# Performance work log

Hardware: AMD Instinct MI355X
Metric: run time of the kernel (lower is better)

## Reference

```python
import jax, jax.numpy as jnp
import numpy as np


def setup_inputs() -> dict:
    key = jax.random.key(0)
    ks = jax.random.split(key, 6)
    B, Din, Dout, K, L = 4096, 4096, 4096, 256, 4
    # scale params like kaiming-ish init to keep activations O(1)
    hin = jax.random.normal(ks[0], (B, Din), dtype=jnp.float32)
    S1s = jax.random.normal(ks[1], (L, Din, K), dtype=jnp.float32) / np.sqrt(Din)
    S2s = jax.random.normal(ks[2], (L, K, Dout), dtype=jnp.float32) / np.sqrt(K)
    U1s = jax.random.normal(ks[3], (L, K, Dout), dtype=jnp.float32) / np.sqrt(K)
    U2s = jax.random.normal(ks[4], (L, Din, K), dtype=jnp.float32) / np.sqrt(Din)
    bias = jax.random.normal(ks[5], (Dout,), dtype=jnp.float32)
    return {"hin": hin, "S1s": S1s, "S2s": S2s, "U1s": U1s, "U2s": U2s, "bias": bias}


def reference(hin, S1s, S2s, U1s, U2s, bias):
    # out = (sum_l (hin @ S1s_l @ U1s_l + hin @ U2s_l @ S2s_l) + bias) / (2 L)
    L = S1s.shape[0]
    a = jnp.einsum('bd,ldk->lbk', hin, S1s)      # [L, B, K]
    t1 = jnp.einsum('lbk,lko->bo', a, U1s)       # [B, Dout]
    b = jnp.einsum('bd,ldk->lbk', hin, U2s)      # [L, B, K]
    t2 = jnp.einsum('lbk,lko->bo', b, S2s)       # [B, Dout]
    return (t1 + t2 + bias) / (2.0 * L)
```

## Files before the change

### kernel.cpp

```cpp
#include <hip/hip_runtime.h>
#include <stdint.h>

typedef unsigned short u16;
typedef __bf16 bf16x8 __attribute__((ext_vector_type(8)));
typedef float f32x4 __attribute__((ext_vector_type(4)));

#define DIN 4096
#define DOUT 4096
#define BB 4096
#define KR 256
#define RK 2048

__device__ __forceinline__ u16 f2bf(float f) {
    union { float f; unsigned u; } v; v.f = f;
    unsigned r = v.u + 0x7FFFu + ((v.u >> 16) & 1u);
    return (u16)(r >> 16);
}

__device__ __forceinline__ void gl_lds16(const void* g, void* l) {
    __builtin_amdgcn_global_load_lds((const __attribute__((address_space(1))) void*)g,
                                     (__attribute__((address_space(3))) void*)l,
                                     16, 0, 0);
}

__global__ __launch_bounds__(256) void cvt_f32_bf16(const float* __restrict__ src,
                                                    u16* __restrict__ dst, int n8) {
    int i = blockIdx.x * blockDim.x + threadIdx.x;
    if (i >= n8) return;
    const float4* s = reinterpret_cast<const float4*>(src) + (size_t)i * 2;
    float4 a = s[0], b = s[1];
    uint4 o;
    o.x = f2bf(a.x) | ((unsigned)f2bf(a.y) << 16);
    o.y = f2bf(a.z) | ((unsigned)f2bf(a.w) << 16);
    o.z = f2bf(b.x) | ((unsigned)f2bf(b.y) << 16);
    o.w = f2bf(b.z) | ((unsigned)f2bf(b.w) << 16);
    reinterpret_cast<uint4*>(dst)[i] = o;
}

__global__ __launch_bounds__(256) void pack_w1t(const float* __restrict__ S1s,
                                                const float* __restrict__ U2s,
                                                u16* __restrict__ W1T) {
    __shared__ u16 lds[64][68];
    int b  = blockIdx.x;
    int bd = b & 63;
    int bk = (b >> 6) & 3;
    int lb = b >> 8;
    int l = lb >> 1, br = lb & 1;
    const float* src = (br ? U2s : S1s) + (size_t)l * DIN * KR;
    int t = threadIdx.x;
    int d0 = bd * 64, k0 = bk * 64;
    int r0 = l * 512 + br * 256 + k0;
    #pragma unroll
    for (int p = 0; p < 4; ++p) {
        int dl = p * 16 + (t >> 4);
        int kc = (t & 15) * 4;
        float4 v = *reinterpret_cast<const float4*>(src + (size_t)(d0 + dl) * KR + k0 + kc);
        ushort4 pk;
        pk.x = f2bf(v.x); pk.y = f2bf(v.y); pk.z = f2bf(v.z); pk.w = f2bf(v.w);
        *reinterpret_cast<ushort4*>(&lds[dl][kc]) = pk;
    }
    __syncthreads();
    #pragma unroll
    for (int p = 0; p < 2; ++p) {
        int kl = p * 32 + (t >> 3);
        int d8 = t & 7;
        u16 tmp[8];
        #pragma unroll
        for (int j = 0; j < 8; ++j) tmp[j] = lds[d8 * 8 + j][kl];
        uint4 o;
        o.x = tmp[0] | ((unsigned)tmp[1] << 16);
        o.y = tmp[2] | ((unsigned)tmp[3] << 16);
        o.z = tmp[4] | ((unsigned)tmp[5] << 16);
        o.w = tmp[6] | ((unsigned)tmp[7] << 16);
        *reinterpret_cast<uint4*>(W1T + (size_t)(r0 + kl) * DIN + d0 + d8 * 8) = o;
    }
}

__global__ __launch_bounds__(256) void pack_w2t(const float* __restrict__ U1s,
                                                const float* __restrict__ S2s,
                                                u16* __restrict__ W2T) {
    __shared__ u16 lds[64][68];
    int b  = blockIdx.x;
    int bo = b & 63;
    int bk = (b >> 6) & 3;
    int lb = b >> 8;
    int l = lb >> 1, br = lb & 1;
    const float* src = (br ? S2s : U1s) + (size_t)l * KR * DOUT;
    int t = threadIdx.x;
    int o0 = bo * 64, k0 = bk * 64;
    #pragma unroll
    for (int p = 0; p < 4; ++p) {
        int kl = p * 16 + (t >> 4);
        int ol = (t & 15) * 4;
        float4 v = *reinterpret_cast<const float4*>(src + (size_t)(k0 + kl) * DOUT + o0 + ol);
        ushort4 pk;
        pk.x = f2bf(v.x); pk.y = f2bf(v.y); pk.z = f2bf(v.z); pk.w = f2bf(v.w);
        *reinterpret_cast<ushort4*>(&lds[kl][ol]) = pk;
    }
    __syncthreads();
    #pragma unroll
    for (int p = 0; p < 2; ++p) {
        int ol = p * 32 + (t >> 3);
        int k8 = t & 7;
        u16 tmp[8];
        #pragma unroll
        for (int j = 0; j < 8; ++j) tmp[j] = lds[k8 * 8 + j][ol];
        uint4 o;
        o.x = tmp[0] | ((unsigned)tmp[1] << 16);
        o.y = tmp[2] | ((unsigned)tmp[3] << 16);
        o.z = tmp[4] | ((unsigned)tmp[5] << 16);
        o.w = tmp[6] | ((unsigned)tmp[7] << 16);
        *reinterpret_cast<uint4*>(W2T + (size_t)(o0 + ol) * RK + l * 512 + br * 256 + k0 + k8 * 8) = o;
    }
}

template <int BN, int EPI>
__global__ __launch_bounds__(512) void gemm8(const u16* __restrict__ A,
                                             const u16* __restrict__ Bt,
                                             void* __restrict__ Cv,
                                             const float* __restrict__ bias,
                                             int N, int Kd) {
    extern __shared__ char smem[];
    constexpr int BHB = (BN == 256) ? 16384 : 8192;
    constexpr int BROWS = BN / 2;
    constexpr int NF = BN / 128;
    char* ldsA = smem;
    char* ldsB = smem + 65536;

    const int tid = threadIdx.x;
    const int l = tid & 63;
    const int wv = tid >> 6;
    const int wr = wv >> 2;
    const int wc = wv & 3;

    int bid = blockIdx.x;
    bid = (bid & 7) * 32 + (bid >> 3);
    const int mt = bid >> 4, nt = bid & 15;
    const int m0 = mt * 256, n0 = nt * BN;

    const int NITER = Kd >> 7;

    size_t aoff[2], boff[2];
    {
        #pragma unroll
        for (int r = 0; r < 2; ++r) {
            int lin = (r * 512 + tid) * 16;
            int s = lin ^ (((lin >> 7) & 7) << 4);
            int e = s >> 1;
            size_t o = (size_t)(e >> 6) * Kd + (e & 63);
            aoff[r] = (size_t)m0 * Kd + o;
            boff[r] = (size_t)n0 * Kd + o;
        }
    }

    auto issueA = [&](int h, int b, size_t kb) {
        char* d = ldsA + (((b << 1) | h) * 16384) + tid * 16;
        gl_lds16(A + aoff[0] + (size_t)h * 128 * Kd + kb, d);
        gl_lds16(A + aoff[1] + (size_t)h * 128 * Kd + kb, d + 8192);
    };
    auto issueB = [&](int h, int b, size_t kb) {
        char* d = ldsB + (((b << 1) | h) * BHB) + tid * 16;
        gl_lds16(Bt + boff[0] + (size_t)h * BROWS * Kd + kb, d);
        if constexpr (BN == 256)
            gl_lds16(Bt + boff[1] + (size_t)h * BROWS * Kd + kb, d + 8192);
    };

    int rowAb[4];
    #pragma unroll
    for (int m = 0; m < 4; ++m) rowAb[m] = (wr * 64 + m * 16 + (l & 15)) * 128;
    int rowBb[NF];
    #pragma unroll
    for (int n = 0; n < NF; ++n)
        rowBb[n] = ((BN == 256 ? wc * 32 : wc * 16) + n * 16 + (l & 15)) * 128;
    const int cc0 = ((l >> 4) ^ (l & 7)) << 4;

    f32x4 acc[2][2][4][NF] = {};

#define PHASE(BUF, MH, NH, ISSUE_STMT, VM) do {                                   \
    bf16x8 af_[4][2]; bf16x8 bq_[NF][2];                                          \
    const char* Ah_ = ldsA + (((BUF) << 1) | (MH)) * 16384;                       \
    const char* Bh_ = ldsB + (((BUF) << 1) | (NH)) * BHB;                         \
    _Pragma("unroll") for (int m_ = 0; m_ < 4; ++m_) {                            \
        af_[m_][0] = *(const bf16x8*)(Ah_ + (rowAb[m_] | cc0));                   \
        af_[m_][1] = *(const bf16x8*)(Ah_ + ((rowAb[m_] | cc0) ^ 64)); }          \
    _Pragma("unroll") for (int n_ = 0; n_ < NF; ++n_) {                           \
        bq_[n_][0] = *(const bf16x8*)(Bh_ + (rowBb[n_] | cc0));                   \
        bq_[n_][1] = *(const bf16x8*)(Bh_ + ((rowBb[n_] | cc0) ^ 64)); }          \
    ISSUE_STMT;                                                                   \
    __builtin_amdgcn_s_barrier();                                                 \
    asm volatile("s_waitcnt lgkmcnt(0)" ::: "memory");                            \
    __builtin_amdgcn_s_setprio(1);                                                \
    _Pragma("unroll") for (int m_ = 0; m_ < 4; ++m_)                              \
        _Pragma("unroll") for (int n_ = 0; n_ < NF; ++n_) {                       \
            acc[MH][NH][m_][n_] = __builtin_amdgcn_mfma_f32_16x16x32_bf16(        \
                af_[m_][0], bq_[n_][0], acc[MH][NH][m_][n_], 0, 0, 0);            \
            acc[MH][NH][m_][n_] = __builtin_amdgcn_mfma_f32_16x16x32_bf16(        \
                af_[m_][1], bq_[n_][1], acc[MH][NH][m_][n_], 0, 0, 0); }          \
    __builtin_amdgcn_s_setprio(0);                                                \
    if (VM) { if (BN == 256) asm volatile("s_waitcnt vmcnt(4)" ::: "memory");     \
              else           asm volatile("s_waitcnt vmcnt(3)" ::: "memory"); }   \
    __builtin_amdgcn_s_barrier();                                                 \
} while (0)

    issueA(0, 0, 0);  issueB(0, 0, 0);
    issueA(1, 0, 0);  issueB(1, 0, 0);
    issueA(0, 1, 64); issueB(0, 1, 64);
    if (BN == 256) asm volatile("s_waitcnt vmcnt(4)" ::: "memory");
    else           asm volatile("s_waitcnt vmcnt(3)" ::: "memory");
    __builtin_amdgcn_s_barrier();

    for (int J = 0; J < NITER; ++J) {
        const size_t kc = (size_t)J << 7;
        PHASE(0, 0, 0, issueA(1, 1, kc + 64),  0);
        PHASE(0, 0, 1, issueB(1, 1, kc + 64),  0);
        PHASE(0, 1, 0, issueA(0, 0, kc + 128), 0);
        PHASE(0, 1, 1, issueB(0, 0, kc + 128), 1);
        PHASE(1, 0, 0, issueA(1, 0, kc + 128), 0);
        PHASE(1, 0, 1, issueB(1, 0, kc + 128), 0);
        PHASE(1, 1, 0, issueA(0, 1, kc + 192), 0);
        PHASE(1, 1, 1, issueB(0, 1, kc + 192), 1);
    }
#undef PHASE

    const int colc = l & 15, rb = (l >> 4) * 4;
    #pragma unroll
    for (int mh = 0; mh < 2; ++mh)
    #pragma unroll
    for (int nh = 0; nh < 2; ++nh)
    #pragma unroll
    for (int m = 0; m < 4; ++m)
    #pragma unroll
    for (int n = 0; n < NF; ++n) {
        int c = n0 + nh * (BN / 2) + wc * (BN / 8) + n * 16 + colc;
        int r0r = m0 + mh * 128 + wr * 64 + m * 16 + rb;
        if (EPI == 0) {
            u16* Cb = (u16*)Cv;
            #pragma unroll
            for (int j = 0; j < 4; ++j)
                Cb[(size_t)(r0r + j) * N + c] = f2bf(acc[mh][nh][m][n][j]);
        } else {
            float* Cf = (float*)Cv;
            float bv = bias[c];
            #pragma unroll
            for (int j = 0; j < 4; ++j)
                Cf[(size_t)(r0r + j) * N + c] = (acc[mh][nh][m][n][j] + bv) * 0.125f;
        }
    }
}

extern "C" void kernel_launch(void* const* d_in, const int* in_sizes, int n_in,
                              void* d_out, int out_size, void* d_ws, size_t ws_size,
                              hipStream_t stream) {
    const float* hin  = (const float*)d_in[0];
    const float* S1s  = (const float*)d_in[1];
    const float* S2s  = (const float*)d_in[2];
    const float* U1s  = (const float*)d_in[3];
    const float* U2s  = (const float*)d_in[4];
    const float* bias = (const float*)d_in[5];
    float* out = (float*)d_out;

    const size_t SZ_HIN = (size_t)BB * DIN * 2 + 512;
    const size_t SZ_W   = (size_t)RK * DIN * 2 + 512;
    const size_t SZ_A   = (size_t)BB * RK * 2 + 512;
    if (ws_size < SZ_HIN + SZ_W + SZ_A) return;
    u16* hinbf = (u16*)d_ws;
    u16* Wx    = (u16*)((char*)d_ws + SZ_HIN);
    u16* abf   = (u16*)((char*)d_ws + SZ_HIN + SZ_W);

    (void)hipFuncSetAttribute(reinterpret_cast<const void*>(&gemm8<128, 0>),
                              hipFuncAttributeMaxDynamicSharedMemorySize, 98304);
    (void)hipFuncSetAttribute(reinterpret_cast<const void*>(&gemm8<256, 1>),
                              hipFuncAttributeMaxDynamicSharedMemorySize, 131072);

    pack_w1t<<<64 * 4 * 8, 256, 0, stream>>>(S1s, U2s, Wx);
    cvt_f32_bf16<<<(BB * DIN / 8) / 256, 256, 0, stream>>>(hin, hinbf, BB * DIN / 8);
    gemm8<128, 0><<<256, 512, 98304, stream>>>(hinbf, Wx, abf, nullptr, RK, DIN);
    pack_w2t<<<64 * 4 * 8, 256, 0, stream>>>(U1s, S2s, Wx);
    gemm8<256, 1><<<256, 512, 131072, stream>>>(abf, Wx, out, bias, DOUT, RK);
}
```

Measured before the change: 189.0 us.

## Reshape wave tiling and reuse A/B LDS fragments across consecutive phases

Makes the per-wave layout configurable (MW waves along M) so each wave computes a tile 2 fragments wide in N. Fragment registers are hoisted out of the phase so A fragments are reused across the two N-halves and B fragments across the M-halves. The phase order is changed to 00,01,11,10 so consecutive phases share one operand. This cuts LDS read traffic per MFMA but raises register pressure, since B fragments for both N-halves stay live.

```diff
diff --git a/kernel.cpp b/kernel.cpp
--- a/kernel.cpp
+++ b/kernel.cpp
@@ -114,7 +114,7 @@
     }
 }
 
-template <int BN, int EPI>
+template <int BN, int MW, int EPI>
 __global__ __launch_bounds__(512) void gemm8(const u16* __restrict__ A,
                                              const u16* __restrict__ Bt,
                                              void* __restrict__ Cv,
@@ -123,15 +123,17 @@
     extern __shared__ char smem[];
     constexpr int BHB = (BN == 256) ? 16384 : 8192;
     constexpr int BROWS = BN / 2;
-    constexpr int NF = BN / 128;
+    constexpr int NW = 8 / MW;
+    constexpr int MF = 128 / (16 * MW);
+    constexpr int MROW = 128 / MW;
     char* ldsA = smem;
     char* ldsB = smem + 65536;
 
     const int tid = threadIdx.x;
     const int l = tid & 63;
     const int wv = tid >> 6;
-    const int wr = wv >> 2;
-    const int wc = wv & 3;
+    const int wr = wv / NW;
+    const int wc = wv % NW;
 
     int bid = blockIdx.x;
     bid = (bid & 7) * 32 + (bid >> 3);
@@ -165,37 +167,37 @@
             gl_lds16(Bt + boff[1] + (size_t)h * BROWS * Kd + kb, d + 8192);
     };
 
-    int rowAb[4];
-    #pragma unroll
-    for (int m = 0; m < 4; ++m) rowAb[m] = (wr * 64 + m * 16 + (l & 15)) * 128;
-    int rowBb[NF];
-    #pragma unroll
-    for (int n = 0; n < NF; ++n)
-        rowBb[n] = ((BN == 256 ? wc * 32 : wc * 16) + n * 16 + (l & 15)) * 128;
+    int rowAb[MF];
+    #pragma unroll
+    for (int m = 0; m < MF; ++m) rowAb[m] = (wr * MROW + m * 16 + (l & 15)) * 128;
+    int rowBb[2];
+    #pragma unroll
+    for (int n = 0; n < 2; ++n) rowBb[n] = (wc * 32 + n * 16 + (l & 15)) * 128;
     const int cc0 = ((l >> 4) ^ (l & 7)) << 4;
 
-    f32x4 acc[2][2][4][NF] = {};
-
-#define PHASE(BUF, MH, NH, ISSUE_STMT, VM) do {                                   \
-    bf16x8 af_[4][2]; bf16x8 bq_[NF][2];                                          \
+    f32x4 acc[2][2][MF][2] = {};
+    bf16x8 af[MF][2];
+    bf16x8 bf[2][2][2];
+
+#define PHASE(BUF, MH, NH, RDA, RDB, ISSUE_STMT, VM) do {                         \
     const char* Ah_ = ldsA + (((BUF) << 1) | (MH)) * 16384;                       \
     const char* Bh_ = ldsB + (((BUF) << 1) | (NH)) * BHB;                         \
-    _Pragma("unroll") for (int m_ = 0; m_ < 4; ++m_) {                            \
-        af_[m_][0] = *(const bf16x8*)(Ah_ + (rowAb[m_] | cc0));                   \
-        af_[m_][1] = *(const bf16x8*)(Ah_ + ((rowAb[m_] | cc0) ^ 64)); }          \
-    _Pragma("unroll") for (int n_ = 0; n_ < NF; ++n_) {                           \
-        bq_[n_][0] = *(const bf16x8*)(Bh_ + (rowBb[n_] | cc0));                   \
-        bq_[n_][1] = *(const bf16x8*)(Bh_ + ((rowBb[n_] | cc0) ^ 64)); }          \
+    if (RDA) { _Pragma("unroll") for (int m_ = 0; m_ < MF; ++m_) {                \
+        af[m_][0] = *(const bf16x8*)(Ah_ + (rowAb[m_] | cc0));                    \
+        af[m_][1] = *(const bf16x8*)(Ah_ + ((rowAb[m_] | cc0) ^ 64)); } }         \
+    if (RDB) { _Pragma("unroll") for (int n_ = 0; n_ < 2; ++n_) {                 \
+        bf[NH][n_][0] = *(const bf16x8*)(Bh_ + (rowBb[n_] | cc0));                \
+        bf[NH][n_][1] = *(const bf16x8*)(Bh_ + ((rowBb[n_] | cc0) ^ 64)); } }     \
     ISSUE_STMT;                                                                   \
     __builtin_amdgcn_s_barrier();                                                 \
     asm volatile("s_waitcnt lgkmcnt(0)" ::: "memory");                            \
     __builtin_amdgcn_s_setprio(1);                                                \
-    _Pragma("unroll") for (int m_ = 0; m_ < 4; ++m_)                              \
-        _Pragma("unroll") for (int n_ = 0; n_ < NF; ++n_) {                       \
+    _Pragma("unroll") for (int m_ = 0; m_ < MF; ++m_)                             \
+        _Pragma("unroll") for (int n_ = 0; n_ < 2; ++n_) {                        \
             acc[MH][NH][m_][n_] = __builtin_amdgcn_mfma_f32_16x16x32_bf16(        \
-                af_[m_][0], bq_[n_][0], acc[MH][NH][m_][n_], 0, 0, 0);            \
+                af[m_][0], bf[NH][n_][0], acc[MH][NH][m_][n_], 0, 0, 0);          \
             acc[MH][NH][m_][n_] = __builtin_amdgcn_mfma_f32_16x16x32_bf16(        \
-                af_[m_][1], bq_[n_][1], acc[MH][NH][m_][n_], 0, 0, 0); }          \
+                af[m_][1], bf[NH][n_][1], acc[MH][NH][m_][n_], 0, 0, 0); }        \
     __builtin_amdgcn_s_setprio(0);                                                \
     if (VM) { if (BN == 256) asm volatile("s_waitcnt vmcnt(4)" ::: "memory");     \
               else           asm volatile("s_waitcnt vmcnt(3)" ::: "memory"); }   \
@@ -211,14 +213,14 @@
 
     for (int J = 0; J < NITER; ++J) {
         const size_t kc = (size_t)J << 7;
-        PHASE(0, 0, 0, issueA(1, 1, kc + 64),  0);
-        PHASE(0, 0, 1, issueB(1, 1, kc + 64),  0);
-        PHASE(0, 1, 0, issueA(0, 0, kc + 128), 0);
-        PHASE(0, 1, 1, issueB(0, 0, kc + 128), 1);
-        PHASE(1, 0, 0, issueA(1, 0, kc + 128), 0);
-        PHASE(1, 0, 1, issueB(1, 0, kc + 128), 0);
-        PHASE(1, 1, 0, issueA(0, 1, kc + 192), 0);
-        PHASE(1, 1, 1, issueB(0, 1, kc + 192), 1);
+        PHASE(0, 0, 0, 1, 1, issueA(1, 1, kc + 64),  0);
+        PHASE(0, 0, 1, 0, 1, issueB(1, 1, kc + 64),  0);
+        PHASE(0, 1, 1, 1, 0, issueA(0, 0, kc + 128), 0);
+        PHASE(0, 1, 0, 0, 0, issueB(0, 0, kc + 128), 1);
+        PHASE(1, 0, 0, 1, 1, issueA(1, 0, kc + 128), 0);
+        PHASE(1, 0, 1, 0, 1, issueB(1, 0, kc + 128), 0);
+        PHASE(1, 1, 1, 1, 0, issueA(0, 1, kc + 192), 0);
+        PHASE(1, 1, 0, 0, 0, issueB(0, 1, kc + 192), 1);
     }
 #undef PHASE
 
@@ -228,11 +230,11 @@
     #pragma unroll
     for (int nh = 0; nh < 2; ++nh)
     #pragma unroll
-    for (int m = 0; m < 4; ++m)
-    #pragma unroll
-    for (int n = 0; n < NF; ++n) {
-        int c = n0 + nh * (BN / 2) + wc * (BN / 8) + n * 16 + colc;
-        int r0r = m0 + mh * 128 + wr * 64 + m * 16 + rb;
+    for (int m = 0; m < MF; ++m)
+    #pragma unroll
+    for (int n = 0; n < 2; ++n) {
+        int c = n0 + nh * (BN / 2) + wc * 32 + n * 16 + colc;
+        int r0r = m0 + mh * 128 + wr * MROW + m * 16 + rb;
         if (EPI == 0) {
             u16* Cb = (u16*)Cv;
             #pragma unroll
@@ -267,14 +269,14 @@
     u16* Wx    = (u16*)((char*)d_ws + SZ_HIN);
     u16* abf   = (u16*)((char*)d_ws + SZ_HIN + SZ_W);
 
-    (void)hipFuncSetAttribute(reinterpret_cast<const void*>(&gemm8<128, 0>),
+    (void)hipFuncSetAttribute(reinterpret_cast<const void*>(&gemm8<128, 4, 0>),
                               hipFuncAttributeMaxDynamicSharedMemorySize, 98304);
-    (void)hipFuncSetAttribute(reinterpret_cast<const void*>(&gemm8<256, 1>),
+    (void)hipFuncSetAttribute(reinterpret_cast<const void*>(&gemm8<256, 2, 1>),
                               hipFuncAttributeMaxDynamicSharedMemorySize, 131072);
 
     pack_w1t<<<64 * 4 * 8, 256, 0, stream>>>(S1s, U2s, Wx);
     cvt_f32_bf16<<<(BB * DIN / 8) / 256, 256, 0, stream>>>(hin, hinbf, BB * DIN / 8);
-    gemm8<128, 0><<<256, 512, 98304, stream>>>(hinbf, Wx, abf, nullptr, RK, DIN);
+    gemm8<128, 4, 0><<<256, 512, 98304, stream>>>(hinbf, Wx, abf, nullptr, RK, DIN);
     pack_w2t<<<64 * 4 * 8, 256, 0, stream>>>(U1s, S2s, Wx);
-    gemm8<256, 1><<<256, 512, 131072, stream>>>(abf, Wx, out, bias, DOUT, RK);
-}
+    gemm8<256, 2, 1><<<256, 512, 131072, stream>>>(abf, Wx, out, bias, DOUT, RK);
+}
```

Result: faster. 169.1 us (-10.5%).
